# Performance work log

Measured on AMD Instinct MI355X. Metric: run time of the kernel, lower is better.

## Reference

```python
import jax, jax.numpy as jnp
import numpy as np

IN_DIM = 128
OUT_DIM = 128
ORDER = 3
N_GRID = 16
KNOTS = jnp.linspace(-1.0, 1.0, N_GRID)  # matches init_kwargs knots
BATCH = 8192


def _extend_grid(grid, order):
    # uniform extension by `order` knots on each side (standard KAN grid extension)
    h = (grid[-1] - grid[0]) / (grid.shape[0] - 1)
    left = grid[0] + h * jnp.arange(-order, 0)
    right = grid[-1] + h * jnp.arange(1, order + 1)
    return jnp.concatenate([left, grid, right])  # [n_grid + 2*order]


def _bspline_basis(x, grid, order):
    # Cox-de-Boor recursion, vectorized over all leading dims of x.
    # returns [..., n_grid + order - 1] degree-`order` B-spline basis values
    g = _extend_grid(grid, order)
    xe = x[..., None]
    B = ((xe >= g[:-1]) & (xe < g[1:])).astype(x.dtype)  # degree 0
    for k in range(1, order + 1):
        left = (xe - g[: -(k + 1)]) / (g[k:-1] - g[: -(k + 1)])
        right = (g[k + 1 :] - xe) / (g[k + 1 :] - g[1:-k])
        B = left * B[..., :-1] + right * B[..., 1:]
    return B


def setup_inputs() -> dict:
    key = jax.random.key(0)
    k1, k2 = jax.random.split(key)
    x = jax.random.normal(k1, (BATCH, IN_DIM), dtype=jnp.float32)
    # coef param: init normal(stddev=0.5), shape (size, n_grid + order - 1)
    coef = 0.5 * jax.random.normal(k2, (OUT_DIM * IN_DIM, N_GRID + ORDER - 1), dtype=jnp.float32)
    return {"x": x, "coef": coef}


def reference(x, coef):
    # full_output: tile x over out_dim, eval spline at tanh(x), residual tanh(x),
    # scales = 1 (non-trainable defaults), dropout inactive, then mean over in_dim.
    xt = jnp.tanh(x)                                   # [B, in]
    basis = _bspline_basis(xt, KNOTS, ORDER)           # [B, in, nb]
    cf = coef.reshape(OUT_DIM, IN_DIM, -1)             # [out, in, nb]
    spline = jnp.einsum('bik,oik->boi', basis, cf)     # [B, out, in]
    y = xt[:, None, :] + spline                        # resid_scale*tanh(x) + spline_scale*spline
    return jnp.mean(y, axis=-1)                        # [B, out]
```

## Files before the change

kernel.cpp:

```cpp
#include <hip/hip_runtime.h>

#define BATCH 8192
#define IN 128
#define OUT 128
#define NB 18
#define ROW (IN * NB)
#define CF_ELEMS (OUT * ROW)
#define MT 32
#define NCHG 4

typedef short  bf16x8 __attribute__((ext_vector_type(8)));
typedef float  f32x16 __attribute__((ext_vector_type(16)));

static __device__ __forceinline__ unsigned short f2bf(float f) {
    union { float f; unsigned u; } v; v.f = f;
    unsigned r = v.u + 0x7fffu + ((v.u >> 16) & 1u);
    return (unsigned short)(r >> 16);
}
static __device__ __forceinline__ bf16x8 as_bf16x8(uint4 v) {
    union { uint4 u; bf16x8 b; } x; x.u = v; return x.b;
}
static __device__ __forceinline__ float fast_tanh(float v) {
    float e = __expf(2.0f * v);
    return 1.0f - 2.0f * __builtin_amdgcn_rcpf(e + 1.0f);
}

__global__ __launch_bounds__(256) void cvt_kernel(const float* __restrict__ cf,
                                                  unsigned short* __restrict__ cfb2) {
    int tid = blockIdx.x * 256 + threadIdx.x;
    int o  = tid & 127;
    int kb = tid >> 7;
    const float4* src = (const float4*)(cf + o * ROW + kb * 8);
    float4 a = src[0], b = src[1];
    uint4 pk;
    pk.x = (unsigned)f2bf(a.x) | ((unsigned)f2bf(a.y) << 16);
    pk.y = (unsigned)f2bf(a.z) | ((unsigned)f2bf(a.w) << 16);
    pk.z = (unsigned)f2bf(b.x) | ((unsigned)f2bf(b.y) << 16);
    pk.w = (unsigned)f2bf(b.z) | ((unsigned)f2bf(b.w) << 16);
    ((uint4*)cfb2)[tid] = pk;
}

__global__ __launch_bounds__(512, 2) void kan_mfma(const float* __restrict__ x,
                                                   const unsigned short* __restrict__ cfb2,
                                                   float* __restrict__ out) {
    __shared__ unsigned sAT[2][3][36][128];
    __shared__ float sbuf[MT][132];
    __shared__ float s_xsp[2][MT];

    const int t  = threadIdx.x;
    const int g  = t >> 8;
    const int tg = t & 255;
    const int w4 = (t >> 6) & 3;
    const int l  = t & 63;
    const int b0 = blockIdx.x * MT;
    const int n0 = w4 << 5;
    const int ab = tg >> 3;
    const int iq = tg & 7;
    const int h  = l >> 5;
    const int am = l & 31;

    {
        const float4* xp = (const float4*)(x + b0 * IN);
        int i0 = t;
        *(float4*)&sbuf[i0 >> 5][(i0 & 31) << 2] = xp[i0];
        int i1 = t + 512;
        *(float4*)&sbuf[i1 >> 5][(i1 & 31) << 2] = xp[i1];
    }
    __syncthreads();

    f32x16 accA, accB;
    #pragma unroll
    for (int r = 0; r < 16; ++r) { accA[r] = 0.f; accB[r] = 0.f; }
    float xs = 0.f;

    const uint4* bbase = (const uint4*)cfb2;
    const int o = n0 + am;

    auto build = [&](int c, int nb) {
        unsigned* tile = &sAT[g][nb][0][0];
        #pragma unroll
        for (int hh = 0; hh < 2; ++hh) {
            int il = iq + (hh << 3);
            int i  = (c << 4) + il;
            float xt = fast_tanh(sbuf[ab][i]);
            xs += xt;
            float s = (xt + 1.0f) * 7.5f;
            int m = (int)s; m = m < 0 ? 0 : (m > 14 ? 14 : m);
            float u = s - (float)m, om = 1.f - u, u2 = u * u;
            float w0 = (1.f / 6.f) * om * om * om;
            float w1 = (2.f / 3.f) - u2 * (1.f - 0.5f * u);
            float w2 = (1.f / 6.f) + 0.5f * (u + u2 - u2 * u);
            float w3 = (1.f / 6.f) * u * u2;
            unsigned lo = (unsigned)f2bf(w0) | ((unsigned)f2bf(w1) << 16);
            unsigned hi = (unsigned)f2bf(w2) | ((unsigned)f2bf(w3) << 16);
            int odd = m & 1;
            unsigned t0 = odd ? (lo << 16) : lo;
            unsigned t1 = odd ? ((hi << 16) | (lo >> 16)) : hi;
            unsigned t2 = odd ? (hi >> 16) : 0u;
            int dq = m >> 1;
            int d0 = il * 9;
            #pragma unroll
            for (int j = 0; j < 9; ++j) {
                int d = d0 + j;
                unsigned v = (j == dq) ? t0 : (j == dq + 1) ? t1
                           : (j == dq + 2) ? t2 : 0u;
                tile[((d >> 2) << 7) + (ab << 2) + (d & 3)] = v;
            }
        }
    };

    build(g * NCHG, 0);

    #pragma unroll
    for (int cc = 0; cc < NCHG; ++cc) {
        const int c = g * NCHG + cc;
        uint4 B[18];
        #pragma unroll
        for (int s = 0; s < 18; ++s)
            B[s] = bbase[(c * 36 + 2 * s + h) * 128 + o];
        if (cc + 1 < NCHG) build(c + 1, (cc + 1) % 3);
        __syncthreads();
        const unsigned* tb = &sAT[g][cc % 3][0][0];
        #pragma unroll
        for (int s = 0; s < 18; ++s) {
            uint4 av = *(const uint4*)(tb + (((2 * s + h) << 7) + (am << 2)));
            if (s & 1) accB = __builtin_amdgcn_mfma_f32_32x32x16_bf16(
                                  as_bf16x8(av), as_bf16x8(B[s]), accB, 0, 0, 0);
            else       accA = __builtin_amdgcn_mfma_f32_32x32x16_bf16(
                                  as_bf16x8(av), as_bf16x8(B[s]), accA, 0, 0, 0);
        }
    }

    #pragma unroll
    for (int r = 0; r < 16; ++r) accA[r] += accB[r];

    xs += __shfl_down(xs, 4, 8);
    xs += __shfl_down(xs, 2, 8);
    xs += __shfl_down(xs, 1, 8);
    if (iq == 0) s_xsp[g][ab] = xs;

    if (g == 1) {
        #pragma unroll
        for (int r = 0; r < 16; ++r) {
            int row = (r & 3) + ((r >> 2) << 3) + (h << 2);
            sbuf[row][n0 + am] = accA[r];
        }
    }
    __syncthreads();
    if (g == 0) {
        #pragma unroll
        for (int r = 0; r < 16; ++r) {
            int row = (r & 3) + ((r >> 2) << 3) + (h << 2);
            float v = accA[r] + sbuf[row][n0 + am] + s_xsp[0][row] + s_xsp[1][row];
            out[(b0 + row) * OUT + n0 + am] = v * (1.0f / 128.0f);
        }
    }
}

__global__ __launch_bounds__(256, 2) void kan_valu(const float* __restrict__ x,
                                                   const float* __restrict__ cf,
                                                   float* __restrict__ out) {
    __shared__ float4        s_w[16][IN];
    __shared__ unsigned char s_m[16][IN];
    __shared__ float         s_xs[16];
    const int t = threadIdx.x;
    const int boff = blockIdx.x * 16;
    {
        const int b = t >> 4, il = t & 15;
        float xs = 0.f;
        #pragma unroll
        for (int k = 0; k < IN / 16; ++k) {
            int i = il + 16 * k;
            float xt = tanhf(x[(boff + b) * IN + i]);
            xs += xt;
            float s = (xt + 1.0f) * 7.5f;
            int m = (int)s; m = m < 0 ? 0 : (m > 14 ? 14 : m);
            float u = s - (float)m, om = 1.f - u, u2 = u * u;
            s_w[b][i] = make_float4((1.f/6.f)*om*om*om,
                                    (2.f/3.f) - u2*(1.f - 0.5f*u),
                                    (1.f/6.f) + 0.5f*(u + u2 - u2*u),
                                    (1.f/6.f)*u*u2);
            s_m[b][i] = (unsigned char)m;
        }
        for (int d = 8; d > 0; d >>= 1) xs += __shfl_down(xs, d, 16);
        if (il == 0) s_xs[b] = xs;
    }
    __syncthreads();
    const int w = t >> 6, l = t & 63;
    #pragma unroll
    for (int r = 0; r < 4; ++r) {
        const int b = w * 4 + r;
        float a0 = 0.f, a1 = 0.f;
        for (int i = 0; i < IN; ++i) {
            float4 wv = s_w[b][i];
            int m = (int)s_m[b][i];
            const float* p0 = cf + (2 * l) * ROW + i * NB + m;
            const float* p1 = p0 + ROW;
            a0 += wv.x * p0[0] + wv.y * p0[1] + wv.z * p0[2] + wv.w * p0[3];
            a1 += wv.x * p1[0] + wv.y * p1[1] + wv.z * p1[2] + wv.w * p1[3];
        }
        float xsv = s_xs[b];
        float2 st; st.x = (xsv + a0) / 128.f; st.y = (xsv + a1) / 128.f;
        ((float2*)out)[(boff + b) * (OUT / 2) + l] = st;
    }
}

extern "C" void kernel_launch(void* const* d_in, const int* in_sizes, int n_in,
                              void* d_out, int out_size, void* d_ws, size_t ws_size,
                              hipStream_t stream) {
    const float* x  = (const float*)d_in[0];
    const float* cf = (const float*)d_in[1];
    float* out = (float*)d_out;
    if (ws_size >= (size_t)CF_ELEMS * sizeof(unsigned short)) {
        unsigned short* cfb2 = (unsigned short*)d_ws;
        cvt_kernel<<<CF_ELEMS / 8 / 256, 256, 0, stream>>>(cf, cfb2);
        kan_mfma<<<BATCH / MT, 512, 0, stream>>>(x, cfb2, out);
    } else {
        kan_valu<<<BATCH / 16, 256, 0, stream>>>(x, cf, out);
    }
}
```

Measured before the change: 69.16 us.

## Fuse coefficient conversion into MFMA kernel via cooperative grid sync

Merges the bf16 coefficient conversion kernel into the main MFMA kernel. Each of the 256 blocks converts a slice of the coefficients, builds its first basis tile, then waits at a cooperative-groups grid barrier before reading the converted weights. This removes one kernel launch and lets the conversion overlap the x load and first tile build. In exchange it adds a grid-wide barrier and depends on all blocks being co-resident, with a fallback to the two-kernel path if the cooperative launch fails.

```diff
diff --git a/kernel.cpp b/kernel.cpp
--- a/kernel.cpp
+++ b/kernel.cpp
@@ -1,4 +1,5 @@
 #include <hip/hip_runtime.h>
+#include <hip/hip_cooperative_groups.h>
 
 #define BATCH 8192
 #define IN 128
@@ -8,6 +9,8 @@
 #define CF_ELEMS (OUT * ROW)
 #define MT 32
 #define NCHG 4
+#define NBLK (BATCH / MT)
+#define CVT_PER_BLK (CF_ELEMS / 8 / NBLK)
 
 typedef short  bf16x8 __attribute__((ext_vector_type(8)));
 typedef float  f32x16 __attribute__((ext_vector_type(16)));
@@ -25,24 +28,10 @@
     return 1.0f - 2.0f * __builtin_amdgcn_rcpf(e + 1.0f);
 }
 
-__global__ __launch_bounds__(256) void cvt_kernel(const float* __restrict__ cf,
-                                                  unsigned short* __restrict__ cfb2) {
-    int tid = blockIdx.x * 256 + threadIdx.x;
-    int o  = tid & 127;
-    int kb = tid >> 7;
-    const float4* src = (const float4*)(cf + o * ROW + kb * 8);
-    float4 a = src[0], b = src[1];
-    uint4 pk;
-    pk.x = (unsigned)f2bf(a.x) | ((unsigned)f2bf(a.y) << 16);
-    pk.y = (unsigned)f2bf(a.z) | ((unsigned)f2bf(a.w) << 16);
-    pk.z = (unsigned)f2bf(b.x) | ((unsigned)f2bf(b.y) << 16);
-    pk.w = (unsigned)f2bf(b.z) | ((unsigned)f2bf(b.w) << 16);
-    ((uint4*)cfb2)[tid] = pk;
-}
-
-__global__ __launch_bounds__(512, 2) void kan_mfma(const float* __restrict__ x,
-                                                   const unsigned short* __restrict__ cfb2,
-                                                   float* __restrict__ out) {
+__global__ __launch_bounds__(512, 2) void kan_fused(const float* __restrict__ x,
+                                                    const float* __restrict__ cf,
+                                                    unsigned short* __restrict__ cfb2,
+                                                    float* __restrict__ out) {
     __shared__ unsigned sAT[2][3][36][128];
     __shared__ float sbuf[MT][132];
     __shared__ float s_xsp[2][MT];
@@ -58,6 +47,20 @@
     const int iq = tg & 7;
     const int h  = l >> 5;
     const int am = l & 31;
+
+    if (t < CVT_PER_BLK) {
+        int idx = blockIdx.x * CVT_PER_BLK + t;
+        int o  = idx & 127;
+        int kb = idx >> 7;
+        const float4* src = (const float4*)(cf + o * ROW + kb * 8);
+        float4 a = src[0], b = src[1];
+        uint4 pk;
+        pk.x = (unsigned)f2bf(a.x) | ((unsigned)f2bf(a.y) << 16);
+        pk.y = (unsigned)f2bf(a.z) | ((unsigned)f2bf(a.w) << 16);
+        pk.z = (unsigned)f2bf(b.x) | ((unsigned)f2bf(b.y) << 16);
+        pk.w = (unsigned)f2bf(b.z) | ((unsigned)f2bf(b.w) << 16);
+        ((uint4*)cfb2)[idx] = pk;
+    }
 
     {
         const float4* xp = (const float4*)(x + b0 * IN);
@@ -111,6 +114,142 @@
 
     build(g * NCHG, 0);
 
+    __threadfence();
+    cooperative_groups::this_grid().sync();
+    __threadfence();
+
+    #pragma unroll
+    for (int cc = 0; cc < NCHG; ++cc) {
+        const int c = g * NCHG + cc;
+        uint4 B[18];
+        #pragma unroll
+        for (int s = 0; s < 18; ++s)
+            B[s] = bbase[(c * 36 + 2 * s + h) * 128 + o];
+        if (cc + 1 < NCHG) build(c + 1, (cc + 1) % 3);
+        __syncthreads();
+        const unsigned* tb = &sAT[g][cc % 3][0][0];
+        #pragma unroll
+        for (int s = 0; s < 18; ++s) {
+            uint4 av = *(const uint4*)(tb + (((2 * s + h) << 7) + (am << 2)));
+            if (s & 1) accB = __builtin_amdgcn_mfma_f32_32x32x16_bf16(
+                                  as_bf16x8(av), as_bf16x8(B[s]), accB, 0, 0, 0);
+            else       accA = __builtin_amdgcn_mfma_f32_32x32x16_bf16(
+                                  as_bf16x8(av), as_bf16x8(B[s]), accA, 0, 0, 0);
+        }
+    }
+
+    #pragma unroll
+    for (int r = 0; r < 16; ++r) accA[r] += accB[r];
+
+    xs += __shfl_down(xs, 4, 8);
+    xs += __shfl_down(xs, 2, 8);
+    xs += __shfl_down(xs, 1, 8);
+    if (iq == 0) s_xsp[g][ab] = xs;
+
+    if (g == 1) {
+        #pragma unroll
+        for (int r = 0; r < 16; ++r) {
+            int row = (r & 3) + ((r >> 2) << 3) + (h << 2);
+            sbuf[row][n0 + am] = accA[r];
+        }
+    }
+    __syncthreads();
+    if (g == 0) {
+        #pragma unroll
+        for (int r = 0; r < 16; ++r) {
+            int row = (r & 3) + ((r >> 2) << 3) + (h << 2);
+            float v = accA[r] + sbuf[row][n0 + am] + s_xsp[0][row] + s_xsp[1][row];
+            out[(b0 + row) * OUT + n0 + am] = v * (1.0f / 128.0f);
+        }
+    }
+}
+
+__global__ __launch_bounds__(256) void cvt_kernel(const float* __restrict__ cf,
+                                                  unsigned short* __restrict__ cfb2) {
+    int tid = blockIdx.x * 256 + threadIdx.x;
+    int o  = tid & 127;
+    int kb = tid >> 7;
+    const float4* src = (const float4*)(cf + o * ROW + kb * 8);
+    float4 a = src[0], b = src[1];
+    uint4 pk;
+    pk.x = (unsigned)f2bf(a.x) | ((unsigned)f2bf(a.y) << 16);
+    pk.y = (unsigned)f2bf(a.z) | ((unsigned)f2bf(a.w) << 16);
+    pk.z = (unsigned)f2bf(b.x) | ((unsigned)f2bf(b.y) << 16);
+    pk.w = (unsigned)f2bf(b.z) | ((unsigned)f2bf(b.w) << 16);
+    ((uint4*)cfb2)[tid] = pk;
+}
+
+__global__ __launch_bounds__(512, 2) void kan_mfma(const float* __restrict__ x,
+                                                   const unsigned short* __restrict__ cfb2,
+                                                   float* __restrict__ out) {
+    __shared__ unsigned sAT[2][3][36][128];
+    __shared__ float sbuf[MT][132];
+    __shared__ float s_xsp[2][MT];
+
+    const int t  = threadIdx.x;
+    const int g  = t >> 8;
+    const int tg = t & 255;
+    const int w4 = (t >> 6) & 3;
+    const int l  = t & 63;
+    const int b0 = blockIdx.x * MT;
+    const int n0 = w4 << 5;
+    const int ab = tg >> 3;
+    const int iq = tg & 7;
+    const int h  = l >> 5;
+    const int am = l & 31;
+
+    {
+        const float4* xp = (const float4*)(x + b0 * IN);
+        int i0 = t;
+        *(float4*)&sbuf[i0 >> 5][(i0 & 31) << 2] = xp[i0];
+        int i1 = t + 512;
+        *(float4*)&sbuf[i1 >> 5][(i1 & 31) << 2] = xp[i1];
+    }
+    __syncthreads();
+
+    f32x16 accA, accB;
+    #pragma unroll
+    for (int r = 0; r < 16; ++r) { accA[r] = 0.f; accB[r] = 0.f; }
+    float xs = 0.f;
+
+    const uint4* bbase = (const uint4*)cfb2;
+    const int o = n0 + am;
+
+    auto build = [&](int c, int nb) {
+        unsigned* tile = &sAT[g][nb][0][0];
+        #pragma unroll
+        for (int hh = 0; hh < 2; ++hh) {
+            int il = iq + (hh << 3);
+            int i  = (c << 4) + il;
+            float xt = fast_tanh(sbuf[ab][i]);
+            xs += xt;
+            float s = (xt + 1.0f) * 7.5f;
+            int m = (int)s; m = m < 0 ? 0 : (m > 14 ? 14 : m);
+            float u = s - (float)m, om = 1.f - u, u2 = u * u;
+            float w0 = (1.f / 6.f) * om * om * om;
+            float w1 = (2.f / 3.f) - u2 * (1.f - 0.5f * u);
+            float w2 = (1.f / 6.f) + 0.5f * (u + u2 - u2 * u);
+            float w3 = (1.f / 6.f) * u * u2;
+            unsigned lo = (unsigned)f2bf(w0) | ((unsigned)f2bf(w1) << 16);
+            unsigned hi = (unsigned)f2bf(w2) | ((unsigned)f2bf(w3) << 16);
+            int odd = m & 1;
+            unsigned t0 = odd ? (lo << 16) : lo;
+            unsigned t1 = odd ? ((hi << 16) | (lo >> 16)) : hi;
+            unsigned t2 = odd ? (hi >> 16) : 0u;
+            int dq = m >> 1;
+            int d0 = il * 9;
+            #pragma unroll
+            for (int j = 0; j < 9; ++j) {
+                int d = d0 + j;
+                unsigned v = (j == dq) ? t0 : (j == dq + 1) ? t1
+                           : (j == dq + 2) ? t2 : 0u;
+                tile[((d >> 2) << 7) + (ab << 2) + (d & 3)] = v;
+            }
+        }
+    };
+
+    build(g * NCHG, 0);
+
     #pragma unroll
     for (int cc = 0; cc < NCHG; ++cc) {
         const int c = g * NCHG + cc;
@@ -213,8 +352,15 @@
     float* out = (float*)d_out;
     if (ws_size >= (size_t)CF_ELEMS * sizeof(unsigned short)) {
         unsigned short* cfb2 = (unsigned short*)d_ws;
-        cvt_kernel<<<CF_ELEMS / 8 / 256, 256, 0, stream>>>(cf, cfb2);
-        kan_mfma<<<BATCH / MT, 512, 0, stream>>>(x, cfb2, out);
+        void* args[] = { (void*)&x, (void*)&cf, (void*)&cfb2, (void*)&out };
+        hipError_t e = hipLaunchCooperativeKernel((const void*)kan_fused,
+                                                  dim3(NBLK), dim3(512),
+                                                  args, 0, stream);
+        if (e != hipSuccess) {
+            (void)hipGetLastError();
+            cvt_kernel<<<CF_ELEMS / 8 / 256, 256, 0, stream>>>(cf, cfb2);
+            kan_mfma<<<BATCH / MT, 512, 0, stream>>>(x, cfb2, out);
+        }
     } else {
         kan_valu<<<BATCH / 16, 256, 0, stream>>>(x, cf, out);
     }
```

Result: slower. 176.3 us (+155.0%).

## Fuse fp32-to-bf16 coefficient conversion into the MFMA kernel, dropping the separate pass

Applied to the files above, without the earlier changes.

Removes the separate conversion kernel and workspace buffer. The main MFMA kernel now reads fp32 coefficients directly and packs them to bf16 with v_cvt_pk_bf16_f32 in registers. This saves a kernel launch and the write/read of the converted buffer. In exchange, every block reloads twice as many bytes with a lane-strided access pattern. The VALU fallback path is also deleted.

```diff
diff --git a/kernel.cpp b/kernel.cpp
--- a/kernel.cpp
+++ b/kernel.cpp
@@ -5,18 +5,12 @@
 #define OUT 128
 #define NB 18
 #define ROW (IN * NB)
-#define CF_ELEMS (OUT * ROW)
 #define MT 32
 #define NCHG 4
 
 typedef short  bf16x8 __attribute__((ext_vector_type(8)));
 typedef float  f32x16 __attribute__((ext_vector_type(16)));
 
-static __device__ __forceinline__ unsigned short f2bf(float f) {
-    union { float f; unsigned u; } v; v.f = f;
-    unsigned r = v.u + 0x7fffu + ((v.u >> 16) & 1u);
-    return (unsigned short)(r >> 16);
-}
 static __device__ __forceinline__ bf16x8 as_bf16x8(uint4 v) {
     union { uint4 u; bf16x8 b; } x; x.u = v; return x.b;
 }
@@ -24,25 +18,20 @@
     float e = __expf(2.0f * v);
     return 1.0f - 2.0f * __builtin_amdgcn_rcpf(e + 1.0f);
 }
-
-__global__ __launch_bounds__(256) void cvt_kernel(const float* __restrict__ cf,
-                                                  unsigned short* __restrict__ cfb2) {
-    int tid = blockIdx.x * 256 + threadIdx.x;
-    int o  = tid & 127;
-    int kb = tid >> 7;
-    const float4* src = (const float4*)(cf + o * ROW + kb * 8);
-    float4 a = src[0], b = src[1];
-    uint4 pk;
-    pk.x = (unsigned)f2bf(a.x) | ((unsigned)f2bf(a.y) << 16);
-    pk.y = (unsigned)f2bf(a.z) | ((unsigned)f2bf(a.w) << 16);
-    pk.z = (unsigned)f2bf(b.x) | ((unsigned)f2bf(b.y) << 16);
-    pk.w = (unsigned)f2bf(b.z) | ((unsigned)f2bf(b.w) << 16);
-    ((uint4*)cfb2)[tid] = pk;
+static __device__ __forceinline__ unsigned short f2bf(float f) {
+    union { float f; unsigned u; } v; v.f = f;
+    unsigned r = v.u + 0x7fffu + ((v.u >> 16) & 1u);
+    return (unsigned short)(r >> 16);
+}
+static __device__ __forceinline__ unsigned cvtpk(float lo, float hi) {
+    unsigned r;
+    asm("v_cvt_pk_bf16_f32 %0, %1, %2" : "=v"(r) : "v"(lo), "v"(hi));
+    return r;
 }
 
-__global__ __launch_bounds__(512, 2) void kan_mfma(const float* __restrict__ x,
-                                                   const unsigned short* __restrict__ cfb2,
-                                                   float* __restrict__ out) {
+__global__ __launch_bounds__(512, 2) void kan_fused(const float* __restrict__ x,
+                                                    const float* __restrict__ cf,
+                                                    float* __restrict__ out) {
     __shared__ unsigned sAT[2][3][36][128];
     __shared__ float sbuf[MT][132];
     __shared__ float s_xsp[2][MT];
@@ -59,6 +48,9 @@
     const int h  = l >> 5;
     const int am = l & 31;
 
+    const int o = n0 + am;
+    const float* crow = cf + (size_t)o * ROW;
+
     {
         const float4* xp = (const float4*)(x + b0 * IN);
         int i0 = t;
@@ -72,9 +64,6 @@
     #pragma unroll
     for (int r = 0; r < 16; ++r) { accA[r] = 0.f; accB[r] = 0.f; }
     float xs = 0.f;
-
-    const uint4* bbase = (const uint4*)cfb2;
-    const int o = n0 + am;
 
     auto build = [&](int c, int nb) {
         unsigned* tile = &sAT[g][nb][0][0];
@@ -116,8 +105,16 @@
         const int c = g * NCHG + cc;
         uint4 B[18];
         #pragma unroll
-        for (int s = 0; s < 18; ++s)
-            B[s] = bbase[(c * 36 + 2 * s + h) * 128 + o];
+        for (int s = 0; s < 18; ++s) {
+            const float4* p = (const float4*)(crow + (c * 36 + 2 * s + h) * 8);
+            float4 a = p[0], b = p[1];
+            uint4 pk;
+            pk.x = cvtpk(a.x, a.y);
+            pk.y = cvtpk(a.z, a.w);
+            pk.z = cvtpk(b.x, b.y);
+            pk.w = cvtpk(b.z, b.w);
+            B[s] = pk;
+        }
         if (cc + 1 < NCHG) build(c + 1, (cc + 1) % 3);
         __syncthreads();
         const unsigned* tb = &sAT[g][cc % 3][0][0];
@@ -157,65 +154,12 @@
     }
 }
 
-__global__ __launch_bounds__(256, 2) void kan_valu(const float* __restrict__ x,
-                                                   const float* __restrict__ cf,
-                                                   float* __restrict__ out) {
-    __shared__ float4        s_w[16][IN];
-    __shared__ unsigned char s_m[16][IN];
-    __shared__ float         s_xs[16];
-    const int t = threadIdx.x;
-    const int boff = blockIdx.x * 16;
-    {
-        const int b = t >> 4, il = t & 15;
-        float xs = 0.f;
-        #pragma unroll
-        for (int k = 0; k < IN / 16; ++k) {
-            int i = il + 16 * k;
-            float xt = tanhf(x[(boff + b) * IN + i]);
-            xs += xt;
-            float s = (xt + 1.0f) * 7.5f;
-            int m = (int)s; m = m < 0 ? 0 : (m > 14 ? 14 : m);
-            float u = s - (float)m, om = 1.f - u, u2 = u * u;
-            s_w[b][i] = make_float4((1.f/6.f)*om*om*om,
-                                    (2.f/3.f) - u2*(1.f - 0.5f*u),
-                                    (1.f/6.f) + 0.5f*(u + u2 - u2*u),
-                                    (1.f/6.f)*u*u2);
-            s_m[b][i] = (unsigned char)m;
-        }
-        for (int d = 8; d > 0; d >>= 1) xs += __shfl_down(xs, d, 16);
-        if (il == 0) s_xs[b] = xs;
-    }
-    __syncthreads();
-    const int w = t >> 6, l = t & 63;
-    #pragma unroll
-    for (int r = 0; r < 4; ++r) {
-        const int b = w * 4 + r;
-        float a0 = 0.f, a1 = 0.f;
-        for (int i = 0; i < IN; ++i) {
-            float4 wv = s_w[b][i];
-            int m = (int)s_m[b][i];
-            const float* p0 = cf + (2 * l) * ROW + i * NB + m;
-            const float* p1 = p0 + ROW;
-            a0 += wv.x * p0[0] + wv.y * p0[1] + wv.z * p0[2] + wv.w * p0[3];
-            a1 += wv.x * p1[0] + wv.y * p1[1] + wv.z * p1[2] + wv.w * p1[3];
-        }
-        float xsv = s_xs[b];
-        float2 st; st.x = (xsv + a0) / 128.f; st.y = (xsv + a1) / 128.f;
-        ((float2*)out)[(boff + b) * (OUT / 2) + l] = st;
-    }
-}
-
 extern "C" void kernel_launch(void* const* d_in, const int* in_sizes, int n_in,
                               void* d_out, int out_size, void* d_ws, size_t ws_size,
                               hipStream_t stream) {
     const float* x  = (const float*)d_in[0];
     const float* cf = (const float*)d_in[1];
     float* out = (float*)d_out;
-    if (ws_size >= (size_t)CF_ELEMS * sizeof(unsigned short)) {
-        unsigned short* cfb2 = (unsigned short*)d_ws;
-        cvt_kernel<<<CF_ELEMS / 8 / 256, 256, 0, stream>>>(cf, cfb2);
-        kan_mfma<<<BATCH / MT, 512, 0, stream>>>(x, cfb2, out);
-    } else {
-        kan_valu<<<BATCH / 16, 256, 0, stream>>>(x, cf, out);
-    }
+    (void)d_ws; (void)ws_size;
+    kan_fused<<<BATCH / MT, 512, 0, stream>>>(x, cf, out);
 }
```

Measured after the change: 92.75 us. 34.1% more time.

## Split input-dim reduction across four wave groups with 1024-thread blocks

Applied to the files above, without the earlier changes.

The MFMA kernel now uses 1024 threads arranged as four groups of four waves, where before it had two groups. Each group handles a quarter of the input dimension in chunks of 8 inputs, down from 16. This halves per-thread B registers and build work per chunk and raises parallelism per block. In exchange it adds extra serialized LDS reduction stages with more barriers, and launch_bounds(1024,4) may be hard to meet under register and LDS limits.

```diff
diff --git a/kernel.cpp b/kernel.cpp
--- a/kernel.cpp
+++ b/kernel.cpp
@@ -7,7 +7,9 @@
 #define ROW (IN * NB)
 #define CF_ELEMS (OUT * ROW)
 #define MT 32
+#define NG 4
 #define NCHG 4
+#define GRAN 18
 
 typedef short  bf16x8 __attribute__((ext_vector_type(8)));
 typedef float  f32x16 __attribute__((ext_vector_type(16)));
@@ -40,12 +42,12 @@
     ((uint4*)cfb2)[tid] = pk;
 }
 
-__global__ __launch_bounds__(512, 2) void kan_mfma(const float* __restrict__ x,
-                                                   const unsigned short* __restrict__ cfb2,
-                                                   float* __restrict__ out) {
-    __shared__ unsigned sAT[2][3][36][128];
+__global__ __launch_bounds__(1024, 4) void kan_mfma(const float* __restrict__ x,
+                                                    const unsigned short* __restrict__ cfb2,
+                                                    float* __restrict__ out) {
+    __shared__ unsigned sAT[NG][3][GRAN][128];
     __shared__ float sbuf[MT][132];
-    __shared__ float s_xsp[2][MT];
+    __shared__ float s_xsp[NG][MT];
 
     const int t  = threadIdx.x;
     const int g  = t >> 8;
@@ -59,12 +61,12 @@
     const int h  = l >> 5;
     const int am = l & 31;
 
+    const uint4* bbase = (const uint4*)cfb2;
+    const int o = n0 + am;
+
     {
         const float4* xp = (const float4*)(x + b0 * IN);
-        int i0 = t;
-        *(float4*)&sbuf[i0 >> 5][(i0 & 31) << 2] = xp[i0];
-        int i1 = t + 512;
-        *(float4*)&sbuf[i1 >> 5][(i1 & 31) << 2] = xp[i1];
+        *(float4*)&sbuf[t >> 5][(t & 31) << 2] = xp[t];
     }
     __syncthreads();
 
@@ -73,39 +75,33 @@
     for (int r = 0; r < 16; ++r) { accA[r] = 0.f; accB[r] = 0.f; }
     float xs = 0.f;
 
-    const uint4* bbase = (const uint4*)cfb2;
-    const int o = n0 + am;
-
     auto build = [&](int c, int nb) {
         unsigned* tile = &sAT[g][nb][0][0];
-        #pragma unroll
-        for (int hh = 0; hh < 2; ++hh) {
-            int il = iq + (hh << 3);
-            int i  = (c << 4) + il;
-            float xt = fast_tanh(sbuf[ab][i]);
-            xs += xt;
-            float s = (xt + 1.0f) * 7.5f;
-            int m = (int)s; m = m < 0 ? 0 : (m > 14 ? 14 : m);
-            float u = s - (float)m, om = 1.f - u, u2 = u * u;
-            float w0 = (1.f / 6.f) * om * om * om;
-            float w1 = (2.f / 3.f) - u2 * (1.f - 0.5f * u);
-            float w2 = (1.f / 6.f) + 0.5f * (u + u2 - u2 * u);
-            float w3 = (1.f / 6.f) * u * u2;
-            unsigned lo = (unsigned)f2bf(w0) | ((unsigned)f2bf(w1) << 16);
-            unsigned hi = (unsigned)f2bf(w2) | ((unsigned)f2bf(w3) << 16);
-            int odd = m & 1;
-            unsigned t0 = odd ? (lo << 16) : lo;
-            unsigned t1 = odd ? ((hi << 16) | (lo >> 16)) : hi;
-            unsigned t2 = odd ? (hi >> 16) : 0u;
-            int dq = m >> 1;
-            int d0 = il * 9;
-            #pragma unroll
-            for (int j = 0; j < 9; ++j) {
-                int d = d0 + j;
-                unsigned v = (j == dq) ? t0 : (j == dq + 1) ? t1
-                           : (j == dq + 2) ? t2 : 0u;
-                tile[((d >> 2) << 7) + (ab << 2) + (d & 3)] = v;
-            }
+        int il = iq;
+        int i  = (c << 3) + il;
+        float xt = fast_tanh(sbuf[ab][i]);
+        xs += xt;
+        float s = (xt + 1.0f) * 7.5f;
+        int m = (int)s; m = m < 0 ? 0 : (m > 14 ? 14 : m);
+        float u = s - (float)m, om = 1.f - u, u2 = u * u;
+        float w0 = (1.f / 6.f) * om * om * om;
+        float w1 = (2.f / 3.f) - u2 * (1.f - 0.5f * u);
+        float w2 = (1.f / 6.f) + 0.5f * (u + u2 - u2 * u);
+        float w3 = (1.f / 6.f) * u * u2;
+        unsigned lo = (unsigned)f2bf(w0) | ((unsigned)f2bf(w1) << 16);
+        unsigned hi = (unsigned)f2bf(w2) | ((unsigned)f2bf(w3) << 16);
+        int odd = m & 1;
+        unsigned t0 = odd ? (lo << 16) : lo;
+        unsigned t1 = odd ? ((hi << 16) | (lo >> 16)) : hi;
+        unsigned t2 = odd ? (hi >> 16) : 0u;
+        int dq = m >> 1;
+        int d0 = il * 9;
+        #pragma unroll
+        for (int j = 0; j < 9; ++j) {
+            int d = d0 + j;
+            unsigned v = (j == dq) ? t0 : (j == dq + 1) ? t1
+                       : (j == dq + 2) ? t2 : 0u;
+            tile[((d >> 2) << 7) + (ab << 2) + (d & 3)] = v;
         }
     };
 
@@ -114,15 +110,15 @@
     #pragma unroll
     for (int cc = 0; cc < NCHG; ++cc) {
         const int c = g * NCHG + cc;
-        uint4 B[18];
-        #pragma unroll
-        for (int s = 0; s < 18; ++s)
-            B[s] = bbase[(c * 36 + 2 * s + h) * 128 + o];
+        uint4 B[9];
+        #pragma unroll
+        for (int s = 0; s < 9; ++s)
+            B[s] = bbase[(c * GRAN + 2 * s + h) * 128 + o];
         if (cc + 1 < NCHG) build(c + 1, (cc + 1) % 3);
         __syncthreads();
         const unsigned* tb = &sAT[g][cc % 3][0][0];
         #pragma unroll
-        for (int s = 0; s < 18; ++s) {
+        for (int s = 0; s < 9; ++s) {
             uint4 av = *(const uint4*)(tb + (((2 * s + h) << 7) + (am << 2)));
             if (s & 1) accB = __builtin_amdgcn_mfma_f32_32x32x16_bf16(
                                   as_bf16x8(av), as_bf16x8(B[s]), accB, 0, 0, 0);
@@ -139,11 +135,27 @@
     xs += __shfl_down(xs, 1, 8);
     if (iq == 0) s_xsp[g][ab] = xs;
 
+    if (g == 3) {
+        #pragma unroll
+        for (int r = 0; r < 16; ++r) {
+            int row = (r & 3) + ((r >> 2) << 3) + (h << 2);
+            sbuf[row][n0 + am] = accA[r];
+        }
+    }
+    __syncthreads();
+    if (g == 2) {
+        #pragma unroll
+        for (int r = 0; r < 16; ++r) {
+            int row = (r & 3) + ((r >> 2) << 3) + (h << 2);
+            sbuf[row][n0 + am] += accA[r];
+        }
+    }
+    __syncthreads();
     if (g == 1) {
         #pragma unroll
         for (int r = 0; r < 16; ++r) {
             int row = (r & 3) + ((r >> 2) << 3) + (h << 2);
-            sbuf[row][n0 + am] = accA[r];
+            sbuf[row][n0 + am] += accA[r];
         }
     }
     __syncthreads();
@@ -151,7 +163,8 @@
         #pragma unroll
         for (int r = 0; r < 16; ++r) {
             int row = (r & 3) + ((r >> 2) << 3) + (h << 2);
-            float v = accA[r] + sbuf[row][n0 + am] + s_xsp[0][row] + s_xsp[1][row];
+            float v = accA[r] + sbuf[row][n0 + am]
+                    + s_xsp[0][row] + s_xsp[1][row] + s_xsp[2][row] + s_xsp[3][row];
             out[(b0 + row) * OUT + n0 + am] = v * (1.0f / 128.0f);
         }
     }
@@ -214,7 +227,7 @@
     if (ws_size >= (size_t)CF_ELEMS * sizeof(unsigned short)) {
         unsigned short* cfb2 = (unsigned short*)d_ws;
         cvt_kernel<<<CF_ELEMS / 8 / 256, 256, 0, stream>>>(cf, cfb2);
-        kan_mfma<<<BATCH / MT, 512, 0, stream>>>(x, cfb2, out);
+        kan_mfma<<<BATCH / MT, 1024, 0, stream>>>(x, cfb2, out);
     } else {
         kan_valu<<<BATCH / 16, 256, 0, stream>>>(x, cf, out);
     }
```

Measured after the change: 68.61 us. About the same (-0.8%).
